# Optimization experiments

Measured on AMD Instinct MI355X. Metric: run time of the kernel, lower is better.

## Reference

```python
import jax, jax.numpy as jnp
import numpy as np

# SSD-style extra-layer channel pyramid for sample_duration=16 (reconstructed):
CH = [(2048, 512, 1024), (1024, 256, 512), (512, 128, 256)]
DN = ('NCDHW', 'OIDHW', 'NCDHW')
B = 128


def conv3d(x, w, stride=(1, 1, 1), padding='VALID', rhs_dilation=None):
    return jax.lax.conv_general_dilated(
        x, w, window_strides=stride, padding=padding,
        rhs_dilation=rhs_dilation, dimension_numbers=DN)


def setup_inputs() -> dict:
    key = jax.random.key(0)
    ks = iter(jax.random.split(key, 32))
    s = 0.02
    d = {}
    d['x'] = jax.random.normal(next(ks), (B, 2048, 16, 2, 2), jnp.float32)
    d['start_boundaries'] = jax.random.randint(next(ks), (B,), 0, 1000, dtype=jnp.int32)
    # head 0 operates on the backbone feature map directly, kernel (2,2,2)
    d['loc_w0'] = s * jax.random.normal(next(ks), (2, 2048, 2, 2, 2), jnp.float32)
    d['conf_w0'] = s * jax.random.normal(next(ks), (3, 2048, 2, 2, 2), jnp.float32)
    for i, (cin, mid, cout) in enumerate(CH):
        d[f'e{i}_w1'] = s * jax.random.normal(next(ks), (mid, cin, 1, 1, 1), jnp.float32)
        d[f'e{i}_w2'] = s * jax.random.normal(next(ks), (cout, mid, 3, 3, 3), jnp.float32)
        d[f'loc_w{i+1}'] = s * jax.random.normal(next(ks), (2, cout, 2, 2, 2), jnp.float32)
        d[f'conf_w{i+1}'] = s * jax.random.normal(next(ks), (3, cout, 2, 2, 2), jnp.float32)
    return d


def reference(x, start_boundaries, loc_w0, conf_w0,
              e0_w1, e0_w2, loc_w1, conf_w1,
              e1_w1, e1_w2, loc_w2, conf_w2,
              e2_w1, e2_w2, loc_w3, conf_w3):
    del start_boundaries  # only used in test phase
    b = x.shape[0]
    loc_ws = [loc_w0, loc_w1, loc_w2, loc_w3]
    conf_ws = [conf_w0, conf_w1, conf_w2, conf_w3]
    extra = [(e0_w1, e0_w2), (e1_w1, e1_w2), (e2_w1, e2_w2)]
    locs = [conv3d(x, loc_ws[0]).reshape(b, -1)]
    confs = [conv3d(x, conf_ws[0]).reshape(b, -1)]
    h = x
    for i, (w1, w2) in enumerate(extra):
        h = conv3d(h, w1)  # 1x1x1 channel reduce
        # 3x3x3, temporal dilation/stride/padding 2 -> T halves, H/W preserved
        h = conv3d(h, w2, stride=(2, 1, 1),
                   padding=[(2, 2), (1, 1), (1, 1)], rhs_dilation=(2, 1, 1))
        locs.append(conv3d(h, loc_ws[i + 1]).reshape(b, -1))
        confs.append(conv3d(h, conf_ws[i + 1]).reshape(b, -1))
    loc = jnp.concatenate(locs, axis=1).reshape(b, -1, 2)    # [B, 26, 2]
    conf = jnp.concatenate(confs, axis=1).reshape(b, -1, 3)  # [B, 26, 3]
    return (loc, conf)
```

## Files before the change

### kernel.cpp

```cpp
#include <hip/hip_runtime.h>

typedef __bf16 bf16;
typedef bf16 bf16x2 __attribute__((ext_vector_type(2)));
typedef bf16 bf16x8 __attribute__((ext_vector_type(8)));
typedef float f32x4 __attribute__((ext_vector_type(4)));

__device__ __forceinline__ void gload16(const bf16* g, bf16* l) {
  __builtin_amdgcn_global_load_lds((const __attribute__((address_space(1))) void*)g,
                                   (__attribute__((address_space(3))) void*)l, 16, 0, 0);
}

template <bool FULL>
__global__ __launch_bounds__(256) void pack_x(const float* __restrict__ x, bf16* __restrict__ dstbuf) {
  __shared__ float tile[64 * 65];
  const int b = blockIdx.x, cb = blockIdx.y;
  const int t = threadIdx.x;
  const float* src = x + ((size_t)b * 2048 + cb * 64) * 64;
  #pragma unroll
  for (int p = 0; p < 16; ++p) {
    int idx = t + p * 256;
    tile[(idx >> 6) * 65 + (idx & 63)] = src[idx];
  }
  __syncthreads();
  if constexpr (FULL) {
    bf16* dst = dstbuf + (size_t)b * 131072 + cb * 64;
    #pragma unroll
    for (int p = 0; p < 8; ++p) {
      int idx = t + p * 256;
      int dhw = idx >> 5;
      int cl2 = (idx & 31) * 2;
      bf16x2 v;
      v.x = (bf16)tile[cl2 * 65 + dhw];
      v.y = (bf16)tile[(cl2 + 1) * 65 + dhw];
      *(bf16x2*)(dst + (size_t)dhw * 2048 + cl2) = v;
    }
  } else {
    bf16* dst = dstbuf + ((size_t)b * 32) * 2048 + cb * 64;
    const int cl2 = (t & 31) * 2, mr0 = t >> 5;
    #pragma unroll
    for (int p = 0; p < 4; ++p) {
      int mrow = mr0 + p * 8;
      int dd = mrow >> 2, hw = mrow & 3;
      int sdhw = dd * 8 + hw;
      bf16x2 v;
      v.x = (bf16)tile[cl2 * 65 + sdhw];
      v.y = (bf16)tile[(cl2 + 1) * 65 + sdhw];
      *(bf16x2*)(dst + (size_t)mrow * 2048 + cl2) = v;
    }
  }
}

__global__ __launch_bounds__(256) void pack_w0(const float* __restrict__ lw0,
                                               const float* __restrict__ cw0,
                                               bf16* __restrict__ Bh) {
  int idx = blockIdx.x * 256 + threadIdx.x;
  int n = idx >> 13, k = idx & 8191;
  int hw = k >> 11, c = k & 2047;
  float v = 0.f;
  if (n < 10) {
    int kd = n / 5, j = n % 5;
    const float* w = (j < 2) ? (lw0 + j * 16384) : (cw0 + (j - 2) * 16384);
    v = w[c * 8 + kd * 4 + hw];
  }
  Bh[idx] = (bf16)v;
}

__global__ __launch_bounds__(256) void head0_gemm(const bf16* __restrict__ xcl,
                                                  const bf16* __restrict__ Bh,
                                                  float* __restrict__ P) {
  __shared__ bf16 ldsA[64 * 64];
  __shared__ bf16 ldsB[16 * 64];
  const int bm = blockIdx.x, ks = blockIdx.y;
  const int tid = threadIdx.x;
  const int wv = tid >> 6, lane = tid & 63, r = lane & 15, g = lane >> 4;
  f32x4 acc = {0.f, 0.f, 0.f, 0.f};
  for (int k0 = 0; k0 < 1024; k0 += 64) {
    #pragma unroll
    for (int q = 0; q < 2; ++q) {
      int idx = tid + q * 256;
      int row = idx >> 3, cg = idx & 7;
      gload16(xcl + (size_t)(bm * 64 + row) * 8192 + ks * 1024 + k0 + (cg ^ (row & 7)) * 8,
              ldsA + idx * 8);
    }
    if (tid < 128) {
      int row = tid >> 3, cg = tid & 7;
      gload16(Bh + (size_t)row * 8192 + ks * 1024 + k0 + (cg ^ (row & 7)) * 8,
              ldsB + tid * 8);
    }
    __syncthreads();
    #pragma unroll
    for (int ks2 = 0; ks2 < 2; ++ks2) {
      int rowa = wv * 16 + r;
      bf16x8 af = *(const bf16x8*)(ldsA + rowa * 64 + ((ks2 * 4 + g) ^ (rowa & 7)) * 8);
      bf16x8 bf_ = *(const bf16x8*)(ldsB + r * 64 + ((ks2 * 4 + g) ^ (r & 7)) * 8);
      acc = __builtin_amdgcn_mfma_f32_16x16x32_bf16(af, bf_, acc, 0, 0, 0);
    }
    __syncthreads();
  }
  const int m = bm * 64 + wv * 16 + g * 4;
  #pragma unroll
  for (int jr = 0; jr < 4; ++jr)
    P[(size_t)(ks * 2048 + m + jr) * 16 + r] = acc[jr];
}

__global__ __launch_bounds__(128) void head0_combine(const float* __restrict__ P,
                                                     float* __restrict__ out) {
  const int b = blockIdx.x, t = threadIdx.x;
  if (t < 75) {
    int j = t / 15, d = t % 15;
    float s = 0.f;
    #pragma unroll
    for (int ks = 0; ks < 8; ++ks) {
      const float* pb = P + (size_t)(ks * 2048 + b * 16) * 16;
      s += pb[d * 16 + j] + pb[(d + 1) * 16 + 5 + j];
    }
    if (j < 2) out[b * 52 + j * 15 + d] = s;
    else       out[6656 + b * 78 + (j - 2) * 15 + d] = s;
  }
}

__global__ __launch_bounds__(256) void cvt_w1(const float* __restrict__ in, bf16* __restrict__ out, int n8) {
  int i = blockIdx.x * 256 + threadIdx.x;
  if (i < n8) {
    const float4* p = (const float4*)(in + (size_t)i * 8);
    float4 a = p[0], b = p[1];
    bf16x8 v = {(bf16)a.x, (bf16)a.y, (bf16)a.z, (bf16)a.w,
                (bf16)b.x, (bf16)b.y, (bf16)b.z, (bf16)b.w};
    *(bf16x8*)(out + (size_t)i * 8) = v;
  }
}

__global__ __launch_bounds__(256) void pack_w2(const float* __restrict__ w2, bf16* __restrict__ w2p,
                                               int oBase, int cin) {
  __shared__ float tile[64 * 27];
  const int orel = blockIdx.x, cb = blockIdx.y;
  const int o = oBase + orel;
  const float* src = w2 + ((size_t)o * cin + cb * 64) * 27;
  const int t = threadIdx.x;
  for (int idx = t; idx < 1728; idx += 256) tile[idx] = src[idx];
  __syncthreads();
  bf16* dst = w2p + (size_t)orel * 27 * cin + cb * 64;
  for (int idx = t; idx < 1728; idx += 256) {
    int tap = idx >> 6, cl = idx & 63;
    dst[(size_t)tap * cin + cl] = (bf16)tile[cl * 27 + tap];
  }
}

struct GP {
  const bf16* A; const bf16* B; bf16* O;
  int K;
  int ashb, asB, am1, as1, am2, as2;
  int oshb, osB, om1, os1, om2, os2, oOff;
  int lgCv, coutS, oCol0, lgCin;
};

template <int FM, int FN, bool W2M>
__global__ __launch_bounds__(256) void gemm_bf(GP p) {
  constexpr int BM = FM * 32, BN = FN * 32;
  __shared__ bf16 lds[(BM + BN) * 64];
  bf16* ldsA = lds;
  bf16* ldsB = lds + BM * 64;
  const int tid = threadIdx.x;
  const int bm = blockIdx.x, bn = blockIdx.y;

  int aBase[BM / 32], aL[BM / 32];
  #pragma unroll
  for (int q = 0; q < BM / 32; ++q) {
    int idx = tid + q * 256;
    int row = idx >> 3, cg = idx & 7;
    int m = bm * BM + row;
    aBase[q] = (m >> p.ashb) * p.asB + ((m >> 2) & p.am1) * p.as1 + (m & p.am2) * p.as2;
    aL[q] = (cg ^ (row & 7)) * 8;
  }
  int bN[BN / 32], bL[BN / 32];
  #pragma unroll
  for (int q = 0; q < BN / 32; ++q) {
    int idx = tid + q * 256;
    int row = idx >> 3, cg = idx & 7;
    bN[q] = bn * BN + row;
    bL[q] = (cg ^ (row & 7)) * 8;
  }

  const int wv = tid >> 6, wm = wv >> 1, wn = wv & 1;
  const int lane = tid & 63, r = lane & 15, g = lane >> 4;

  f32x4 acc[FM][FN];
  const f32x4 zz = {0.f, 0.f, 0.f, 0.f};
  #pragma unroll
  for (int i = 0; i < FM; ++i)
    #pragma unroll
    for (int j = 0; j < FN; ++j) acc[i][j] = zz;

  for (int k0 = 0; k0 < p.K; k0 += 64) {
    #pragma unroll
    for (int q = 0; q < BM / 32; ++q) {
      int idx = tid + q * 256;
      gload16(p.A + aBase[q] + k0 + aL[q], ldsA + idx * 8);
    }
    if (W2M) {
      const int kd = k0 >> (p.lgCin + 2);
      const int hw = (k0 >> p.lgCin) & 3;
      const int c0 = k0 & ((1 << p.lgCin) - 1);
      #pragma unroll
      for (int q = 0; q < BN / 32; ++q) {
        int n = bN[q];
        int op = n & ((1 << p.lgCv) - 1);
        int hwp = n >> p.lgCv;
        int kh = 1 + (hw >> 1) - (hwp >> 1);
        int kw = 1 + (hw & 1) - (hwp & 1);
        int src = ((op * 27 + kd * 9 + kh * 3 + kw) << p.lgCin) + c0 + bL[q];
        int idx = tid + q * 256;
        gload16(p.B + src, ldsB + idx * 8);
      }
    } else {
      #pragma unroll
      for (int q = 0; q < BN / 32; ++q) {
        int idx = tid + q * 256;
        gload16(p.B + (size_t)bN[q] * p.K + k0 + bL[q], ldsB + idx * 8);
      }
    }
    __syncthreads();
    #pragma unroll
    for (int ks = 0; ks < 2; ++ks) {
      bf16x8 af[FM], bfr[FN];
      #pragma unroll
      for (int i = 0; i < FM; ++i) {
        int row = wm * FM * 16 + i * 16 + r;
        int pcg = (ks * 4 + g) ^ (row & 7);
        af[i] = *(const bf16x8*)(ldsA + row * 64 + pcg * 8);
      }
      #pragma unroll
      for (int j = 0; j < FN; ++j) {
        int row = wn * FN * 16 + j * 16 + r;
        int pcg = (ks * 4 + g) ^ (row & 7);
        bfr[j] = *(const bf16x8*)(ldsB + row * 64 + pcg * 8);
      }
      #pragma unroll
      for (int i = 0; i < FM; ++i)
        #pragma unroll
        for (int j = 0; j < FN; ++j)
          acc[i][j] = __builtin_amdgcn_mfma_f32_16x16x32_bf16(af[i], bfr[j], acc[i][j], 0, 0, 0);
    }
    __syncthreads();
  }

  #pragma unroll
  for (int i = 0; i < FM; ++i) {
    #pragma unroll
    for (int j = 0; j < FN; ++j) {
      int ncol = bn * BN + wn * FN * 16 + j * 16 + r;
      int outcol = (ncol >> p.lgCv) * p.coutS + p.oCol0 + (ncol & ((1 << p.lgCv) - 1));
      #pragma unroll
      for (int jr = 0; jr < 4; ++jr) {
        int m = bm * BM + wm * FM * 16 + i * 16 + g * 4 + jr;
        int oa = (m >> p.oshb) * p.osB + ((m >> 2) & p.om1) * p.os1 + (m & p.om2) * p.os2 + p.oOff + outcol;
        p.O[oa] = (bf16)acc[i][j][jr];
      }
    }
  }
}

template <typename T, bool XL>
__global__ __launch_bounds__(256)
void heads_k(const T* __restrict__ in, const float* __restrict__ wl,
             const float* __restrict__ wc, float* __restrict__ out,
             const int C, const int dcnt, const int sB, const int sD,
             const int sHW, const int sC, const int loff, const int coff) {
  const int tid = threadIdx.x;
  const int blk = blockIdx.x;
  const int b = blk / dcnt, d = blk - b * dcnt;
  float a0 = 0, a1 = 0, c0 = 0, c1 = 0, c2 = 0;
  const int C8 = C * 8;
  if constexpr (XL) {
    const int hw = tid & 3, kd = (tid >> 2) & 1, cb = tid >> 3;
    const int base = b * sB + (d + kd) * sD + hw * sHW;
    const int wb = kd * 4 + hw;
    for (int i = 0; i < C / 32; ++i) {
      const int c = cb + i * 32;
      const float v = (float)in[base + c * sC];
      const int wi = c * 8 + wb;
      a0 += v * wl[wi];  a1 += v * wl[C8 + wi];
      c0 += v * wc[wi];  c1 += v * wc[C8 + wi];  c2 += v * wc[2 * C8 + wi];
    }
  } else {
    for (int c = tid; c < C; c += 256) {
      #pragma unroll
      for (int kd = 0; kd < 2; ++kd) {
        #pragma unroll
        for (int hw = 0; hw < 4; ++hw) {
          const float v = (float)in[b * sB + (d + kd) * sD + hw * sHW + c];
          const int wi = c * 8 + kd * 4 + hw;
          a0 += v * wl[wi];  a1 += v * wl[C8 + wi];
          c0 += v * wc[wi];  c1 += v * wc[C8 + wi];  c2 += v * wc[2 * C8 + wi];
        }
      }
    }
  }
  #pragma unroll
  for (int off = 32; off; off >>= 1) {
    a0 += __shfl_down(a0, off, 64);
    a1 += __shfl_down(a1, off, 64);
    c0 += __shfl_down(c0, off, 64);
    c1 += __shfl_down(c1, off, 64);
    c2 += __shfl_down(c2, off, 64);
  }
  __shared__ float red[5][4];
  const int lane = tid & 63, wv = tid >> 6;
  if (lane == 0) { red[0][wv] = a0; red[1][wv] = a1; red[2][wv] = c0; red[3][wv] = c1; red[4][wv] = c2; }
  __syncthreads();
  if (tid == 0) {
    float L0 = red[0][0] + red[0][1] + red[0][2] + red[0][3];
    float L1 = red[1][0] + red[1][1] + red[1][2] + red[1][3];
    float F0 = red[2][0] + red[2][1] + red[2][2] + red[2][3];
    float F1 = red[3][0] + red[3][1] + red[3][2] + red[3][3];
    float F2 = red[4][0] + red[4][1] + red[4][2] + red[4][3];
    float* loc = out + (size_t)b * 52 + loff;
    loc[0 * dcnt + d] = L0;
    loc[1 * dcnt + d] = L1;
    float* cf = out + 6656 + (size_t)b * 78 + coff;
    cf[0 * dcnt + d] = F0;
    cf[1 * dcnt + d] = F1;
    cf[2 * dcnt + d] = F2;
  }
}

extern "C" void kernel_launch(void* const* d_in, const int* in_sizes, int n_in,
                              void* d_out, int out_size, void* d_ws, size_t ws_size,
                              hipStream_t stream) {
  (void)in_sizes; (void)n_in; (void)out_size;
  const float* x    = (const float*)d_in[0];
  const float* lw0  = (const float*)d_in[2];
  const float* cw0  = (const float*)d_in[3];
  const float* e0w1 = (const float*)d_in[4];
  const float* e0w2 = (const float*)d_in[5];
  const float* lw1  = (const float*)d_in[6];
  const float* cw1  = (const float*)d_in[7];
  const float* e1w1 = (const float*)d_in[8];
  const float* e1w2 = (const float*)d_in[9];
  const float* lw2  = (const float*)d_in[10];
  const float* cw2  = (const float*)d_in[11];
  const float* e2w1 = (const float*)d_in[12];
  const float* e2w2 = (const float*)d_in[13];
  const float* lw3  = (const float*)d_in[14];
  const float* cw3  = (const float*)d_in[15];
  float* out = (float*)d_out;
  bf16* W = (bf16*)d_ws;

  if (ws_size >= (size_t)49283072) {
    const size_t xclo = 0;
    const size_t W1f  = 16777216;
    const size_t h1af = 17825792;
    const size_t h1bf = 20447232;
    const size_t w2p0f = 0;
    const size_t W1c1f = 0, h2af = 262144, w2p1f = 1048576, h2bf = 4587520;
    const size_t W1c2f = 6684672, h3af = 6750208, w2p2f = 7012352, h3bf = 7897088;
    bf16* Bh = W + h1bf;
    float* P = (float*)(W + h1bf + 131072);

    hipMemsetAsync(W + h1af, 0, (size_t)2621440 * 2, stream);
    pack_x<true><<<dim3(128, 32), 256, 0, stream>>>(x, W + xclo);
    pack_w0<<<512, 256, 0, stream>>>(lw0, cw0, Bh);
    head0_gemm<<<dim3(32, 8), 256, 0, stream>>>(W + xclo, Bh, P);
    head0_combine<<<128, 128, 0, stream>>>(P, out);
    cvt_w1<<<512, 256, 0, stream>>>(e0w1, W + W1f, 131072);

    GP g1 = {W + xclo, W + W1f, W + h1af, 2048,
             5, 131072, 7, 16384, 3, 2048,
             5, 20480, 7, 2048, 3, 512, 2048,
             9, 512, 0, 0};
    gemm_bf<2, 2, false><<<dim3(64, 8), 256, 0, stream>>>(g1);

    pack_w2<<<dim3(1024, 8), 256, 0, stream>>>(e0w2, W + w2p0f, 0, 512);
    GP g2 = {W + h1af, W + w2p0f, W + h1bf, 6144,
             3, 20480, 0, 0, 7, 2048,
             0, 4096, 0, 0, 0, 0, 0,
             10, 1024, 0, 9};
    gemm_bf<2, 2, true><<<dim3(16, 64), 256, 0, stream>>>(g2);
    heads_k<bf16, false><<<128 * 7, 256, 0, stream>>>(
        W + h1bf, lw1, cw1, out, 1024, 7, 32768, 4096, 1024, 1, 30, 45);

    hipMemsetAsync(W + h2af, 0, (size_t)786432 * 2, stream);
    cvt_w1<<<128, 256, 0, stream>>>(e1w1, W + W1c1f, 32768);
    GP g3 = {W + h1bf, W + W1c1f, W + h2af, 1024,
             4, 32768, 3, 8192, 3, 1024,
             4, 6144, 3, 1024, 3, 256, 1024,
             8, 256, 0, 0};
    gemm_bf<1, 1, false><<<dim3(64, 8), 256, 0, stream>>>(g3);
    pack_w2<<<dim3(512, 4), 256, 0, stream>>>(e1w2, W + w2p1f, 0, 256);
    GP g4 = {W + h2af, W + w2p1f, W + h2bf, 3072,
             2, 6144, 0, 0, 3, 1024,
             0, 2048, 0, 0, 0, 0, 0,
             9, 512, 0, 8};
    gemm_bf<1, 1, true><<<dim3(16, 64), 256, 0, stream>>>(g4);
    heads_k<bf16, false><<<128 * 3, 256, 0, stream>>>(
        W + h2bf, lw2, cw2, out, 512, 3, 8192, 2048, 512, 1, 44, 66);

    hipMemsetAsync(W + h3af, 0, (size_t)262144 * 2, stream);
    cvt_w1<<<32, 256, 0, stream>>>(e2w1, W + W1c2f, 8192);
    GP g5 = {W + h2bf, W + W1c2f, W + h3af, 512,
             3, 8192, 1, 4096, 3, 512,
             3, 2048, 1, 512, 3, 128, 512,
             7, 128, 0, 0};
    gemm_bf<1, 1, false><<<dim3(32, 4), 256, 0, stream>>>(g5);
    pack_w2<<<dim3(256, 2), 256, 0, stream>>>(e2w2, W + w2p2f, 0, 128);
    GP g6 = {W + h3af, W + w2p2f, W + h3bf, 1536,
             1, 2048, 0, 0, 1, 512,
             0, 1024, 0, 0, 0, 0, 0,
             8, 256, 0, 7};
    gemm_bf<1, 1, true><<<dim3(8, 32), 256, 0, stream>>>(g6);
    heads_k<bf16, false><<<128 * 1, 256, 0, stream>>>(
        W + h3bf, lw3, cw3, out, 256, 1, 2048, 1024, 256, 1, 50, 75);
    return;
  }

  const size_t A0o  = 0;
  const size_t W1o  = 8388608;
  const size_t h1ao = 9437184;
  const size_t h1bo = 12058624;
  const size_t W1c1 = 8388608, W1c2 = 8650752, h3ao = 8716288, h3bo = 8978432;
  const size_t h2ao = 9437184, h2bo = 12058624;
  const size_t w2p0o = 0, w2p1o = 0, w2p2o = 3538944;

  hipMemsetAsync(W + h1ao, 0, (size_t)2621440 * 2, stream);
  pack_x<false><<<dim3(128, 32), 256, 0, stream>>>(x, W + A0o);
  cvt_w1<<<512, 256, 0, stream>>>(e0w1, W + W1o, 131072);

  GP g1 = {W + A0o, W + W1o, W + h1ao, 2048,
           0, 2048, 0, 0, 0, 0,
           5, 20480, 7, 2048, 3, 512, 2048,
           9, 512, 0, 0};
  gemm_bf<2, 2, false><<<dim3(64, 8), 256, 0, stream>>>(g1);

  pack_w2<<<dim3(512, 8), 256, 0, stream>>>(e0w2, W + w2p0o, 0, 512);
  GP g2a = {W + h1ao, W + w2p0o, W + h1bo, 6144,
            3, 20480, 0, 0, 7, 2048,
            0, 4096, 0, 0, 0, 0, 0,
            9, 1024, 0, 9};
  gemm_bf<2, 2, true><<<dim3(16, 32), 256, 0, stream>>>(g2a);
  pack_w2<<<dim3(512, 8), 256, 0, stream>>>(e0w2, W + w2p0o, 512, 512);
  GP g2b = {W + h1ao, W + w2p0o, W + h1bo, 6144,
            3, 20480, 0, 0, 7, 2048,
            0, 4096, 0, 0, 0, 0, 0,
            9, 1024, 512, 9};
  gemm_bf<2, 2, true><<<dim3(16, 32), 256, 0, stream>>>(g2b);

  heads_k<bf16, false><<<128 * 7, 256, 0, stream>>>(
      W + h1bo, lw1, cw1, out, 1024, 7, 32768, 4096, 1024, 1, 30, 45);

  hipMemsetAsync(W + h2ao, 0, (size_t)786432 * 2, stream);
  cvt_w1<<<128, 256, 0, stream>>>(e1w1, W + W1c1, 32768);
  GP g3 = {W + h1bo, W + W1c1, W + h2ao, 1024,
           4, 32768, 3, 8192, 3, 1024,
           4, 6144, 3, 1024, 3, 256, 1024,
           8, 256, 0, 0};
  gemm_bf<1, 1, false><<<dim3(64, 8), 256, 0, stream>>>(g3);
  pack_w2<<<dim3(512, 4), 256, 0, stream>>>(e1w2, W + w2p1o, 0, 256);
  GP g4 = {W + h2ao, W + w2p1o, W + h2bo, 3072,
           2, 6144, 0, 0, 3, 1024,
           0, 2048, 0, 0, 0, 0, 0,
           9, 512, 0, 8};
  gemm_bf<1, 1, true><<<dim3(16, 64), 256, 0, stream>>>(g4);
  heads_k<bf16, false><<<128 * 3, 256, 0, stream>>>(
      W + h2bo, lw2, cw2, out, 512, 3, 8192, 2048, 512, 1, 44, 66);

  hipMemsetAsync(W + h3ao, 0, (size_t)262144 * 2, stream);
  cvt_w1<<<32, 256, 0, stream>>>(e2w1, W + W1c2, 8192);
  GP g5 = {W + h2bo, W + W1c2, W + h3ao, 512,
           3, 8192, 1, 4096, 3, 512,
           3, 2048, 1, 512, 3, 128, 512,
           7, 128, 0, 0};
  gemm_bf<1, 1, false><<<dim3(32, 4), 256, 0, stream>>>(g5);
  pack_w2<<<dim3(256, 2), 256, 0, stream>>>(e2w2, W + w2p2o, 0, 128);
  GP g6 = {W + h3ao, W + w2p2o, W + h3bo, 1536,
           1, 2048, 0, 0, 1, 512,
           0, 1024, 0, 0, 0, 0, 0,
           8, 256, 0, 7};
  gemm_bf<1, 1, true><<<dim3(8, 32), 256, 0, stream>>>(g6);
  heads_k<bf16, false><<<128 * 1, 256, 0, stream>>>(
      W + h3bo, lw3, cw3, out, 256, 1, 2048, 1024, 256, 1, 50, 75);

  heads_k<float, true><<<128 * 15, 256, 0, stream>>>(
      x, lw0, cw0, out, 2048, 15, 131072, 4, 1, 64, 0, 0);
}
```

Measured before the change: 249.0 us.

## Add double-buffered 128x128 GEMM for first 3x3x3 conv and precompute weight offsets

Replaces the generic gemm_bf call for the stage-0 3x3x3 conv with a dedicated gemm2_db kernel. It uses 128x128 tiles, double-buffered LDS, and prefetches the next K-slice while running MFMAs on the current one. The generic kernel's W2M path also moves the per-iteration kh/kw index arithmetic into per-block precomputed offsets. The aim is to hide global-to-LDS load latency and cut address math. The cost is a larger 64KB LDS footprint and fewer blocks per CU, with hardcoded shapes.

```diff
diff --git a/kernel.cpp b/kernel.cpp
--- a/kernel.cpp
+++ b/kernel.cpp
@@ -170,15 +170,32 @@
     int row = idx >> 3, cg = idx & 7;
     int m = bm * BM + row;
     aBase[q] = (m >> p.ashb) * p.asB + ((m >> 2) & p.am1) * p.as1 + (m & p.am2) * p.as2;
-    aL[q] = (cg ^ (row & 7)) * 8;
-  }
+    aL[q] = ((cg ^ row) & 7) * 8;
+  }
+  int opk[BN / 32];
   int bN[BN / 32], bL[BN / 32];
+  int khkw0 = 0, khkw1 = 0, khkw2 = 0, khkw3 = 0;
   #pragma unroll
   for (int q = 0; q < BN / 32; ++q) {
     int idx = tid + q * 256;
     int row = idx >> 3, cg = idx & 7;
-    bN[q] = bn * BN + row;
-    bL[q] = (cg ^ (row & 7)) * 8;
+    int n = bn * BN + row;
+    int sw = ((cg ^ row) & 7) * 8;
+    if constexpr (W2M) {
+      int op = n & ((1 << p.lgCv) - 1);
+      opk[q] = (op * 27 << p.lgCin) + sw;
+      bN[q] = 0; bL[q] = 0;
+    } else {
+      bN[q] = n; bL[q] = sw; opk[q] = 0;
+    }
+  }
+  if constexpr (W2M) {
+    const int hwp = (bn * BN) >> p.lgCv;
+    const int hp = hwp >> 1, wp = hwp & 1;
+    khkw0 = ((1 - hp) * 3 + (1 - wp)) << p.lgCin;
+    khkw1 = ((1 - hp) * 3 + (2 - wp)) << p.lgCin;
+    khkw2 = ((2 - hp) * 3 + (1 - wp)) << p.lgCin;
+    khkw3 = ((2 - hp) * 3 + (2 - wp)) << p.lgCin;
   }
 
   const int wv = tid >> 6, wm = wv >> 1, wn = wv & 1;
@@ -197,20 +214,17 @@
       int idx = tid + q * 256;
       gload16(p.A + aBase[q] + k0 + aL[q], ldsA + idx * 8);
     }
-    if (W2M) {
+    if constexpr (W2M) {
       const int kd = k0 >> (p.lgCin + 2);
-      const int hw = (k0 >> p.lgCin) & 3;
+      const int hwsel = (k0 >> p.lgCin) & 3;
       const int c0 = k0 & ((1 << p.lgCin) - 1);
+      int kk = (hwsel & 2) ? ((hwsel & 1) ? khkw3 : khkw2)
+                           : ((hwsel & 1) ? khkw1 : khkw0);
+      const int koff = (kd * 9 << p.lgCin) + kk + c0;
       #pragma unroll
       for (int q = 0; q < BN / 32; ++q) {
-        int n = bN[q];
-        int op = n & ((1 << p.lgCv) - 1);
-        int hwp = n >> p.lgCv;
-        int kh = 1 + (hw >> 1) - (hwp >> 1);
-        int kw = 1 + (hw & 1) - (hwp & 1);
-        int src = ((op * 27 + kd * 9 + kh * 3 + kw) << p.lgCin) + c0 + bL[q];
         int idx = tid + q * 256;
-        gload16(p.B + src, ldsB + idx * 8);
+        gload16(p.B + opk[q] + koff, ldsB + idx * 8);
       }
     } else {
       #pragma unroll
@@ -255,6 +269,113 @@
         int m = bm * BM + wm * FM * 16 + i * 16 + g * 4 + jr;
         int oa = (m >> p.oshb) * p.osB + ((m >> 2) & p.om1) * p.os1 + (m & p.om2) * p.os2 + p.oOff + outcol;
         p.O[oa] = (bf16)acc[i][j][jr];
+      }
+    }
+  }
+}
+
+__global__ __launch_bounds__(256) void gemm2_db(const bf16* __restrict__ A,
+                                                const bf16* __restrict__ B,
+                                                bf16* __restrict__ O) {
+  __shared__ bf16 lds[2][16384];
+  const int tid = threadIdx.x;
+  const int bm = blockIdx.x, bn = blockIdx.y;
+
+  int aOff[4], bOff[4];
+  #pragma unroll
+  for (int q = 0; q < 4; ++q) {
+    int idx = tid + q * 256;
+    int row = idx >> 3, cg = idx & 7;
+    int sw = ((cg ^ row) & 7) * 8;
+    int m = bm * 128 + row;
+    aOff[q] = (m >> 3) * 20480 + (m & 7) * 2048 + sw;
+    int n = bn * 128 + row;
+    bOff[q] = (n & 1023) * 13824 + sw;
+  }
+  const int hwp = (bn * 128) >> 10;
+  const int hp = hwp >> 1, wp = hwp & 1;
+  const int kk0 = ((1 - hp) * 3 + (1 - wp)) << 9;
+  const int kk1 = ((1 - hp) * 3 + (2 - wp)) << 9;
+  const int kk2 = ((2 - hp) * 3 + (1 - wp)) << 9;
+  const int kk3 = ((2 - hp) * 3 + (2 - wp)) << 9;
+
+  const int wv = tid >> 6, wm = wv >> 1, wn = wv & 1;
+  const int lane = tid & 63, r = lane & 15, g = lane >> 4;
+
+  f32x4 acc[4][4];
+  const f32x4 zz = {0.f, 0.f, 0.f, 0.f};
+  #pragma unroll
+  for (int i = 0; i < 4; ++i)
+    #pragma unroll
+    for (int j = 0; j < 4; ++j) acc[i][j] = zz;
+
+  auto koffOf = [&](int k0) {
+    int kd = k0 >> 11, hws = (k0 >> 9) & 3, c0 = k0 & 511;
+    int kk = (hws & 2) ? ((hws & 1) ? kk3 : kk2) : ((hws & 1) ? kk1 : kk0);
+    return kd * 4608 + kk + c0;
+  };
+
+  {
+    int ko = koffOf(0);
+    #pragma unroll
+    for (int q = 0; q < 4; ++q) {
+      int idx = tid + q * 256;
+      gload16(A + aOff[q], &lds[0][idx * 8]);
+      gload16(B + bOff[q] + ko, &lds[0][8192 + idx * 8]);
+    }
+  }
+  __syncthreads();
+
+  int cur = 0;
+  for (int t = 0; t < 96; ++t) {
+    if (t < 95) {
+      int k1 = (t + 1) * 64;
+      int ko = koffOf(k1);
+      int nb = cur ^ 1;
+      #pragma unroll
+      for (int q = 0; q < 4; ++q) {
+        int idx = tid + q * 256;
+        gload16(A + aOff[q] + k1, &lds[nb][idx * 8]);
+        gload16(B + bOff[q] + ko, &lds[nb][8192 + idx * 8]);
+      }
+    }
+    __builtin_amdgcn_sched_barrier(0);
+    const bf16* LA = lds[cur];
+    const bf16* LB = lds[cur] + 8192;
+    #pragma unroll
+    for (int ks = 0; ks < 2; ++ks) {
+      bf16x8 af[4], bfr[4];
+      #pragma unroll
+      for (int i = 0; i < 4; ++i) {
+        int row = wm * 64 + i * 16 + r;
+        int pcg = (ks * 4 + g) ^ (row & 7);
+        af[i] = *(const bf16x8*)(LA + row * 64 + pcg * 8);
+      }
+      #pragma unroll
+      for (int j = 0; j < 4; ++j) {
+        int row = wn * 64 + j * 16 + r;
+        int pcg = (ks * 4 + g) ^ (row & 7);
+        bfr[j] = *(const bf16x8*)(LB + row * 64 + pcg * 8);
+      }
+      #pragma unroll
+      for (int i = 0; i < 4; ++i)
+        #pragma unroll
+        for (int j = 0; j < 4; ++j)
+          acc[i][j] = __builtin_amdgcn_mfma_f32_16x16x32_bf16(af[i], bfr[j], acc[i][j], 0, 0, 0);
+    }
+    __syncthreads();
+    cur ^= 1;
+  }
+
+  #pragma unroll
+  for (int i = 0; i < 4; ++i) {
+    #pragma unroll
+    for (int j = 0; j < 4; ++j) {
+      int n = bn * 128 + wn * 64 + j * 16 + r;
+      #pragma unroll
+      for (int jr = 0; jr < 4; ++jr) {
+        int m = bm * 128 + wm * 64 + i * 16 + g * 4 + jr;
+        O[(size_t)m * 4096 + n] = (bf16)acc[i][j][jr];
       }
     }
   }
@@ -371,11 +492,7 @@
     gemm_bf<2, 2, false><<<dim3(64, 8), 256, 0, stream>>>(g1);
 
     pack_w2<<<dim3(1024, 8), 256, 0, stream>>>(e0w2, W + w2p0f, 0, 512);
-    GP g2 = {W + h1af, W + w2p0f, W + h1bf, 6144,
-             3, 20480, 0, 0, 7, 2048,
-             0, 4096, 0, 0, 0, 0, 0,
-             10, 1024, 0, 9};
-    gemm_bf<2, 2, true><<<dim3(16, 64), 256, 0, stream>>>(g2);
+    gemm2_db<<<dim3(8, 32), 256, 0, stream>>>(W + h1af, W + w2p0f, W + h1bf);
     heads_k<bf16, false><<<128 * 7, 256, 0, stream>>>(
         W + h1bf, lw1, cw1, out, 1024, 7, 32768, 4096, 1024, 1, 30, 45);
 
```

New measurement: 283.2 us. 13.7% more time.
